# Kernel tuning notes

Measured on AMD Instinct MI355X. Metric: run time of the kernel, lower is better.

The kernel has to match this reference:

```python
import jax, jax.numpy as jnp
import numpy as np

B, D, V = 524288, 64, 1000000

def _prelu(x, a=1.0):
    # F.prelu with weight tensor(1.0) -> identity, but kept explicit for faithfulness
    return jnp.where(x >= 0, x, a * x)

def setup_inputs() -> dict:
    key = jax.random.key(0)
    ks = jax.random.split(key, 10)
    return {
        "nodes": jax.random.randint(ks[0], (B,), 0, V),
        "node2e_weight": jax.random.normal(ks[1], (V, D), jnp.float32) * 0.1,
        "l1neighs_feats": jax.random.normal(ks[2], (B, D), jnp.float32),
        "l2neighs_feats": jax.random.normal(ks[3], (B, D), jnp.float32),
        "alpha_w": jax.random.normal(ks[4], (1, 2 * D), jnp.float32) * 0.05,
        "alpha_b": jax.random.normal(ks[5], (1,), jnp.float32) * 0.05,
        "beta_w": jax.random.normal(ks[6], (1, 2 * D), jnp.float32) * 0.05,
        "beta_b": jax.random.normal(ks[7], (1,), jnp.float32) * 0.05,
        "gamma_w": jax.random.normal(ks[8], (D, D), jnp.float32) * 0.05,
        "gamma_b": jax.random.normal(ks[9], (D,), jnp.float32) * 0.05,
    }

def reference(nodes, node2e_weight, l1neighs_feats, l2neighs_feats,
              alpha_w, alpha_b, beta_w, beta_b, gamma_w, gamma_b):
    # self_feats = node2e.weight[nodes]  -> embedding gather [B, D]
    self_feats = node2e_weight[nodes]
    # dual gates: Linear(2D -> 1) + PReLU(weight=1.0)
    alphaa = _prelu(jnp.concatenate([self_feats, l1neighs_feats], axis=1) @ alpha_w.T + alpha_b)  # [B,1]
    betaa = _prelu(jnp.concatenate([self_feats, l2neighs_feats], axis=1) @ beta_w.T + beta_b)     # [B,1]
    # weighted combine
    combined = self_feats + alphaa * l1neighs_feats + betaa * l2neighs_feats  # [B,D]
    # final Linear(D -> D) + PReLU(weight=1.0)
    return _prelu(combined @ gamma_w.T + gamma_b)
```

## Files before the change

kernel.cpp:

```cpp
#include <hip/hip_runtime.h>

typedef __attribute__((ext_vector_type(8))) short short8;
typedef __attribute__((ext_vector_type(4))) float f32x4;
typedef __attribute__((ext_vector_type(4))) float f4;

__device__ inline float dot4(f4 a, f4 b) { return a.x*b.x + a.y*b.y + a.z*b.z + a.w*b.w; }
__device__ inline f4 comb4(f4 s, float al, f4 x, float be, f4 y) { return s + al*x + be*y; }

__device__ inline short bf16rne(float x) {
    unsigned u = __float_as_uint(x);
    u += 0x7FFFu + ((u >> 16) & 1u);
    return (short)(u >> 16);
}
__device__ inline short8 pack_bf16(f4 a, f4 b) {
    short8 r;
    r[0] = bf16rne(a.x); r[1] = bf16rne(a.y); r[2] = bf16rne(a.z); r[3] = bf16rne(a.w);
    r[4] = bf16rne(b.x); r[5] = bf16rne(b.y); r[6] = bf16rne(b.z); r[7] = bf16rne(b.w);
    return r;
}

struct Feats { f4 w[4]; f4 x[4]; f4 y[4]; };

__global__ __launch_bounds__(256, 1)
void encoder_mfma(const int* __restrict__ nodes,
                  const float* __restrict__ W,
                  const float* __restrict__ L1,
                  const float* __restrict__ L2,
                  const float* __restrict__ AW,
                  const float* __restrict__ ABv,
                  const float* __restrict__ BW,
                  const float* __restrict__ BBv,
                  const float* __restrict__ GW,
                  const float* __restrict__ GB,
                  float* __restrict__ out,
                  int nrows)
{
    const int lane = threadIdx.x & 63;
    const int wid  = threadIdx.x >> 6;
    const int m    = lane & 15;
    const int g    = lane >> 4;

    const int i0 = 2 * g, i1 = 2 * g + 1, i2 = 8 + 2 * g, i3 = 9 + 2 * g;

    const unsigned nGroups = (unsigned)nrows >> 4;
    const unsigned stride  = (unsigned)gridDim.x * 4u;

    short8 gB0[4], gB1[4];
    float  gbv[4];
#pragma unroll
    for (int t = 0; t < 4; ++t) {
        const int n = t * 16 + m;
        const f4* Gp = reinterpret_cast<const f4*>(GW + (unsigned)n * 64u);
        gB0[t] = pack_bf16(Gp[i0], Gp[i1]);
        gB1[t] = pack_bf16(Gp[i2], Gp[i3]);
        gbv[t] = GB[n];
    }
    const float ab = ABv[0], bb = BBv[0];
    const f4* AWp = reinterpret_cast<const f4*>(AW);
    const f4* BWp = reinterpret_cast<const f4*>(BW);

    auto load_feats = [&](int nidx, unsigned grpL) -> Feats {
        Feats F;
        const unsigned row = grpL * 16u + (unsigned)m;
        const f4* Wp  = reinterpret_cast<const f4*>(W + (unsigned)nidx * 64u);
        const f4* L1p = reinterpret_cast<const f4*>(L1 + (size_t)row * 64u);
        const f4* L2p = reinterpret_cast<const f4*>(L2 + (size_t)row * 64u);
        F.w[0] = Wp[i0]; F.w[1] = Wp[i1]; F.w[2] = Wp[i2]; F.w[3] = Wp[i3];
        F.x[0] = __builtin_nontemporal_load(L1p + i0);
        F.x[1] = __builtin_nontemporal_load(L1p + i1);
        F.x[2] = __builtin_nontemporal_load(L1p + i2);
        F.x[3] = __builtin_nontemporal_load(L1p + i3);
        F.y[0] = __builtin_nontemporal_load(L2p + i0);
        F.y[1] = __builtin_nontemporal_load(L2p + i1);
        F.y[2] = __builtin_nontemporal_load(L2p + i2);
        F.y[3] = __builtin_nontemporal_load(L2p + i3);
        return F;
    };

    auto compute_store = [&](const Feats& F, unsigned grpC) {
        const unsigned row0 = grpC * 16u;
        float pa = dot4(F.w[0], AWp[i0]) + dot4(F.w[1], AWp[i1])
                 + dot4(F.w[2], AWp[i2]) + dot4(F.w[3], AWp[i3])
                 + dot4(F.x[0], AWp[16 + i0]) + dot4(F.x[1], AWp[16 + i1])
                 + dot4(F.x[2], AWp[16 + i2]) + dot4(F.x[3], AWp[16 + i3]);
        float pb = dot4(F.w[0], BWp[i0]) + dot4(F.w[1], BWp[i1])
                 + dot4(F.w[2], BWp[i2]) + dot4(F.w[3], BWp[i3])
                 + dot4(F.y[0], BWp[16 + i0]) + dot4(F.y[1], BWp[16 + i1])
                 + dot4(F.y[2], BWp[16 + i2]) + dot4(F.y[3], BWp[16 + i3]);
        pa += __shfl_xor(pa, 16); pa += __shfl_xor(pa, 32);
        pb += __shfl_xor(pb, 16); pb += __shfl_xor(pb, 32);
        const float alpha = pa + ab;
        const float beta  = pb + bb;

        const short8 a0 = pack_bf16(comb4(F.w[0], alpha, F.x[0], beta, F.y[0]),
                                    comb4(F.w[1], alpha, F.x[1], beta, F.y[1]));
        const short8 a1 = pack_bf16(comb4(F.w[2], alpha, F.x[2], beta, F.y[2]),
                                    comb4(F.w[3], alpha, F.x[3], beta, F.y[3]));

        f32x4 acc[4];
#pragma unroll
        for (int t = 0; t < 4; ++t) {
            acc[t][0] = gbv[t]; acc[t][1] = gbv[t]; acc[t][2] = gbv[t]; acc[t][3] = gbv[t];
            acc[t] = __builtin_amdgcn_mfma_f32_16x16x32_bf16(a0, gB0[t], acc[t], 0, 0, 0);
            acc[t] = __builtin_amdgcn_mfma_f32_16x16x32_bf16(a1, gB1[t], acc[t], 0, 0, 0);
        }
#pragma unroll
        for (int t = 0; t < 4; ++t) {
#pragma unroll
            for (int r = 0; r < 4; ++r) {
                out[(row0 + 4u * (unsigned)g + r) * 64u + (unsigned)(t * 16 + m)] = acc[t][r];
            }
        }
    };

    unsigned grp = (unsigned)blockIdx.x * 4u + (unsigned)wid;
    if (grp >= nGroups) return;

    int nvA = nodes[grp * 16u + (unsigned)m];
    Feats A = load_feats(nvA, grp);
    unsigned gn = grp + stride;
    int nvPF = (gn < nGroups) ? nodes[gn * 16u + (unsigned)m] : 0;

    while (true) {
        Feats B;
        const bool hasN = (gn < nGroups);
        if (hasN) {
            B = load_feats(nvPF, gn);
            const unsigned g2 = gn + stride;
            nvA = (g2 < nGroups) ? nodes[g2 * 16u + (unsigned)m] : 0;
        }
        compute_store(A, grp);
        if (!hasN) return;
        grp = gn; gn += stride;

        const bool hasN2 = (gn < nGroups);
        if (hasN2) {
            A = load_feats(nvA, gn);
            const unsigned g2 = gn + stride;
            nvPF = (g2 < nGroups) ? nodes[g2 * 16u + (unsigned)m] : 0;
        }
        compute_store(B, grp);
        if (!hasN2) return;
        grp = gn; gn += stride;
    }
}

extern "C" void kernel_launch(void* const* d_in, const int* in_sizes, int n_in,
                              void* d_out, int out_size, void* d_ws, size_t ws_size,
                              hipStream_t stream) {
    const int*   nodes = (const int*)  d_in[0];
    const float* W     = (const float*)d_in[1];
    const float* L1    = (const float*)d_in[2];
    const float* L2    = (const float*)d_in[3];
    const float* AW    = (const float*)d_in[4];
    const float* AB    = (const float*)d_in[5];
    const float* BW    = (const float*)d_in[6];
    const float* BB    = (const float*)d_in[7];
    const float* GW    = (const float*)d_in[8];
    const float* GB    = (const float*)d_in[9];
    float* out = (float*)d_out;
    const int nrows = in_sizes[0];

    hipLaunchKernelGGL(encoder_mfma, dim3(2048), dim3(256), 0, stream,
                       nodes, W, L1, L2, AW, AB, BW, BB, GW, GB, out, nrows);
}
```

Baseline: 121.9 us.

## Stage embedding gather through LDS via async global_load_lds, raise occupancy

The embedding-row gather now goes asynchronously into a per-wave double-buffered LDS region using global_load_lds, instead of into registers. The gamma weight fragments are re-read and repacked to bf16 on every group rather than held in registers, cutting register pressure so that launch bounds can allow 4 blocks per CU. The grid shrinks from 2048 to 1024 blocks. The intent is more memory-level parallelism for the random gather. The risks are extra per-iteration GW loads and conversions, and missing explicit waits before reading LDS, which could race with the async copies.

Result: slower. 266.3 us (+118.5%).

```diff
diff --git a/kernel.cpp b/kernel.cpp
--- a/kernel.cpp
+++ b/kernel.cpp
@@ -19,9 +19,10 @@
     return r;
 }
 
-struct Feats { f4 w[4]; f4 x[4]; f4 y[4]; };
+#define AS1(p) ((const __attribute__((address_space(1))) void*)(p))
+#define AS3(p) ((__attribute__((address_space(3))) void*)(p))
 
-__global__ __launch_bounds__(256, 1)
+__global__ __launch_bounds__(256, 4)
 void encoder_mfma(const int* __restrict__ nodes,
                   const float* __restrict__ W,
                   const float* __restrict__ L1,
@@ -42,73 +43,75 @@
 
     const int i0 = 2 * g, i1 = 2 * g + 1, i2 = 8 + 2 * g, i3 = 9 + 2 * g;
 
+    __shared__ f4 ldsW[4][2][4][64];
+
     const unsigned nGroups = (unsigned)nrows >> 4;
     const unsigned stride  = (unsigned)gridDim.x * 4u;
 
-    short8 gB0[4], gB1[4];
-    float  gbv[4];
-#pragma unroll
-    for (int t = 0; t < 4; ++t) {
-        const int n = t * 16 + m;
-        const f4* Gp = reinterpret_cast<const f4*>(GW + (unsigned)n * 64u);
-        gB0[t] = pack_bf16(Gp[i0], Gp[i1]);
-        gB1[t] = pack_bf16(Gp[i2], Gp[i3]);
-        gbv[t] = GB[n];
-    }
     const float ab = ABv[0], bb = BBv[0];
     const f4* AWp = reinterpret_cast<const f4*>(AW);
     const f4* BWp = reinterpret_cast<const f4*>(BW);
+    float gbvA[4];
+#pragma unroll
+    for (int t = 0; t < 4; ++t) gbvA[t] = GB[t * 16 + m];
 
-    auto load_feats = [&](int nidx, unsigned grpL) -> Feats {
-        Feats F;
+    auto issueW = [&](int buf, int nidx) {
+        const float* base = W + (unsigned)nidx * 64u;
+        f4* d = &ldsW[wid][buf][0][0];
+        __builtin_amdgcn_global_load_lds(AS1(base + 4 * i0), AS3(d),       16, 0, 0);
+        __builtin_amdgcn_global_load_lds(AS1(base + 4 * i1), AS3(d + 64),  16, 0, 0);
+        __builtin_amdgcn_global_load_lds(AS1(base + 4 * i2), AS3(d + 128), 16, 0, 0);
+        __builtin_amdgcn_global_load_lds(AS1(base + 4 * i3), AS3(d + 192), 16, 0, 0);
+    };
+
+    auto loadStreams = [&](unsigned grpL, f4* x, f4* y) {
         const unsigned row = grpL * 16u + (unsigned)m;
-        const f4* Wp  = reinterpret_cast<const f4*>(W + (unsigned)nidx * 64u);
         const f4* L1p = reinterpret_cast<const f4*>(L1 + (size_t)row * 64u);
         const f4* L2p = reinterpret_cast<const f4*>(L2 + (size_t)row * 64u);
-        F.w[0] = Wp[i0]; F.w[1] = Wp[i1]; F.w[2] = Wp[i2]; F.w[3] = Wp[i3];
-        F.x[0] = __builtin_nontemporal_load(L1p + i0);
-        F.x[1] = __builtin_nontemporal_load(L1p + i1);
-        F.x[2] = __builtin_nontemporal_load(L1p + i2);
-        F.x[3] = __builtin_nontemporal_load(L1p + i3);
-        F.y[0] = __builtin_nontemporal_load(L2p + i0);
-        F.y[1] = __builtin_nontemporal_load(L2p + i1);
-        F.y[2] = __builtin_nontemporal_load(L2p + i2);
-        F.y[3] = __builtin_nontemporal_load(L2p + i3);
-        return F;
+        x[0] = __builtin_nontemporal_load(L1p + i0);
+        x[1] = __builtin_nontemporal_load(L1p + i1);
+        x[2] = __builtin_nontemporal_load(L1p + i2);
+        x[3] = __builtin_nontemporal_load(L1p + i3);
+        y[0] = __builtin_nontemporal_load(L2p + i0);
+        y[1] = __builtin_nontemporal_load(L2p + i1);
+        y[2] = __builtin_nontemporal_load(L2p + i2);
+        y[3] = __builtin_nontemporal_load(L2p + i3);
     };
 
-    auto compute_store = [&](const Feats& F, unsigned grpC) {
-        const unsigned row0 = grpC * 16u;
-        float pa = dot4(F.w[0], AWp[i0]) + dot4(F.w[1], AWp[i1])
-                 + dot4(F.w[2], AWp[i2]) + dot4(F.w[3], AWp[i3])
-                 + dot4(F.x[0], AWp[16 + i0]) + dot4(F.x[1], AWp[16 + i1])
-                 + dot4(F.x[2], AWp[16 + i2]) + dot4(F.x[3], AWp[16 + i3]);
-        float pb = dot4(F.w[0], BWp[i0]) + dot4(F.w[1], BWp[i1])
-                 + dot4(F.w[2], BWp[i2]) + dot4(F.w[3], BWp[i3])
-                 + dot4(F.y[0], BWp[16 + i0]) + dot4(F.y[1], BWp[16 + i1])
-                 + dot4(F.y[2], BWp[16 + i2]) + dot4(F.y[3], BWp[16 + i3]);
+    auto computeRest = [&](f4 w0, f4 w1, f4 w2, f4 w3,
+                           const f4* x, const f4* y, unsigned grpC) {
+        float pa = dot4(w0, AWp[i0]) + dot4(w1, AWp[i1])
+                 + dot4(w2, AWp[i2]) + dot4(w3, AWp[i3])
+                 + dot4(x[0], AWp[16 + i0]) + dot4(x[1], AWp[16 + i1])
+                 + dot4(x[2], AWp[16 + i2]) + dot4(x[3], AWp[16 + i3]);
+        float pb = dot4(w0, BWp[i0]) + dot4(w1, BWp[i1])
+                 + dot4(w2, BWp[i2]) + dot4(w3, BWp[i3])
+                 + dot4(y[0], BWp[16 + i0]) + dot4(y[1], BWp[16 + i1])
+                 + dot4(y[2], BWp[16 + i2]) + dot4(y[3], BWp[16 + i3]);
         pa += __shfl_xor(pa, 16); pa += __shfl_xor(pa, 32);
         pb += __shfl_xor(pb, 16); pb += __shfl_xor(pb, 32);
         const float alpha = pa + ab;
         const float beta  = pb + bb;
 
-        const short8 a0 = pack_bf16(comb4(F.w[0], alpha, F.x[0], beta, F.y[0]),
-                                    comb4(F.w[1], alpha, F.x[1], beta, F.y[1]));
-        const short8 a1 = pack_bf16(comb4(F.w[2], alpha, F.x[2], beta, F.y[2]),
-                                    comb4(F.w[3], alpha, F.x[3], beta, F.y[3]));
+        const short8 a0 = pack_bf16(comb4(w0, alpha, x[0], beta, y[0]),
+                                    comb4(w1, alpha, x[1], beta, y[1]));
+        const short8 a1 = pack_bf16(comb4(w2, alpha, x[2], beta, y[2]),
+                                    comb4(w3, alpha, x[3], beta, y[3]));
 
-        f32x4 acc[4];
+        const unsigned row0 = grpC * 16u;
 #pragma unroll
         for (int t = 0; t < 4; ++t) {
-            acc[t][0] = gbv[t]; acc[t][1] = gbv[t]; acc[t][2] = gbv[t]; acc[t][3] = gbv[t];
-            acc[t] = __builtin_amdgcn_mfma_f32_16x16x32_bf16(a0, gB0[t], acc[t], 0, 0, 0);
-            acc[t] = __builtin_amdgcn_mfma_f32_16x16x32_bf16(a1, gB1[t], acc[t], 0, 0, 0);
-        }
-#pragma unroll
-        for (int t = 0; t < 4; ++t) {
+            const int n = t * 16 + m;
+            const f4* Gp = reinterpret_cast<const f4*>(GW + (unsigned)n * 64u);
+            const short8 b0 = pack_bf16(Gp[i0], Gp[i1]);
+            const short8 b1 = pack_bf16(Gp[i2], Gp[i3]);
+            f32x4 acc;
+            acc[0] = gbvA[t]; acc[1] = gbvA[t]; acc[2] = gbvA[t]; acc[3] = gbvA[t];
+            acc = __builtin_amdgcn_mfma_f32_16x16x32_bf16(a0, b0, acc, 0, 0, 0);
+            acc = __builtin_amdgcn_mfma_f32_16x16x32_bf16(a1, b1, acc, 0, 0, 0);
 #pragma unroll
             for (int r = 0; r < 4; ++r) {
-                out[(row0 + 4u * (unsigned)g + r) * 64u + (unsigned)(t * 16 + m)] = acc[t][r];
+                out[(row0 + 4u * (unsigned)g + r) * 64u + (unsigned)n] = acc[r];
             }
         }
     };
@@ -116,30 +119,41 @@
     unsigned grp = (unsigned)blockIdx.x * 4u + (unsigned)wid;
     if (grp >= nGroups) return;
 
-    int nvA = nodes[grp * 16u + (unsigned)m];
-    Feats A = load_feats(nvA, grp);
+    f4 Ax[4], Ay[4], Bx[4], By[4];
+    int nv = nodes[grp * 16u + (unsigned)m];
+    issueW(0, nv);
+    loadStreams(grp, Ax, Ay);
     unsigned gn = grp + stride;
-    int nvPF = (gn < nGroups) ? nodes[gn * 16u + (unsigned)m] : 0;
+    int nvN = (gn < nGroups) ? nodes[gn * 16u + (unsigned)m] : 0;
 
     while (true) {
-        Feats B;
+        f4 w0 = ldsW[wid][0][0][lane];
+        f4 w1 = ldsW[wid][0][1][lane];
+        f4 w2 = ldsW[wid][0][2][lane];
+        f4 w3 = ldsW[wid][0][3][lane];
         const bool hasN = (gn < nGroups);
         if (hasN) {
-            B = load_feats(nvPF, gn);
+            issueW(1, nvN);
+            loadStreams(gn, Bx, By);
             const unsigned g2 = gn + stride;
-            nvA = (g2 < nGroups) ? nodes[g2 * 16u + (unsigned)m] : 0;
+            nv = (g2 < nGroups) ? nodes[g2 * 16u + (unsigned)m] : 0;
         }
-        compute_store(A, grp);
+        computeRest(w0, w1, w2, w3, Ax, Ay, grp);
         if (!hasN) return;
         grp = gn; gn += stride;
 
+        f4 v0 = ldsW[wid][1][0][lane];
+        f4 v1 = ldsW[wid][1][1][lane];
+        f4 v2 = ldsW[wid][1][2][lane];
+        f4 v3 = ldsW[wid][1][3][lane];
         const bool hasN2 = (gn < nGroups);
         if (hasN2) {
-            A = load_feats(nvA, gn);
+            issueW(0, nv);
+            loadStreams(gn, Ax, Ay);
             const unsigned g2 = gn + stride;
-            nvPF = (g2 < nGroups) ? nodes[g2 * 16u + (unsigned)m] : 0;
+            nvN = (g2 < nGroups) ? nodes[g2 * 16u + (unsigned)m] : 0;
         }
-        compute_store(B, grp);
+        computeRest(v0, v1, v2, v3, Bx, By, grp);
         if (!hasN2) return;
         grp = gn; gn += stride;
     }
@@ -161,6 +175,6 @@
     float* out = (float*)d_out;
     const int nrows = in_sizes[0];
 
-    hipLaunchKernelGGL(encoder_mfma, dim3(2048), dim3(256), 0, stream,
+    hipLaunchKernelGGL(encoder_mfma, dim3(1024), dim3(256), 0, stream,
                        nodes, W, L1, L2, AW, AB, BW, BB, GW, GB, out, nrows);
 }
```
